# Kernel tuning notes

Hardware: AMD Instinct MI355X
Metric: run time of the kernel (lower is better)

The kernel has to match this reference:

```python
import jax, jax.numpy as jnp
import numpy as np

B, N, D, H = 4, 2048, 768, 12
HD = D // H
SCALE = HD ** -0.5


def setup_inputs() -> dict:
    key = jax.random.key(0)
    k1, k2, k3 = jax.random.split(key, 3)
    x = jax.random.normal(k1, (B, N, D), dtype=jnp.float32)
    w_qkv = jax.random.normal(k2, (D, 3 * D), dtype=jnp.float32) * (D ** -0.5)
    w_proj = jax.random.normal(k3, (D, D), dtype=jnp.float32) * (D ** -0.5)
    b_proj = jnp.zeros((D,), dtype=jnp.float32)
    return {"x": x, "w_qkv": w_qkv, "w_proj": w_proj, "b_proj": b_proj}


def reference(x, w_qkv, w_proj, b_proj):
    b, n, d = x.shape
    qkv = x @ w_qkv                      # [b, n, 3d]
    q, k, v = jnp.split(qkv, 3, axis=-1)
    # [b, n, d] -> [b, h, n, hd]
    split_heads = lambda t: t.reshape(b, n, H, HD).transpose(0, 2, 1, 3)
    q, k, v = split_heads(q), split_heads(k), split_heads(v)
    dots = jnp.einsum('bhqd,bhkd->bhqk', q, k) * SCALE   # [b, h, n, n]
    attn = jax.nn.softmax(dots, axis=-1)
    q_attn = attn[:, :, 0, :]            # attention row of query token 0: [b, h, n]
    # dropout p=0 (eval) -> identity
    out = jnp.einsum('bhqk,bhkd->bhqd', attn, v)          # [b, h, n, hd]
    out = out.transpose(0, 2, 1, 3).reshape(b, n, d)      # [b, n, d]
    return out @ w_proj + b_proj, q_attn
```

## Files before the change

kernel.cpp:

```cpp
#include <hip/hip_runtime.h>


typedef unsigned short u16;
typedef __attribute__((ext_vector_type(8))) short bf8;
typedef __attribute__((ext_vector_type(4))) short bf4;
typedef __attribute__((ext_vector_type(4))) int i4;
typedef __attribute__((ext_vector_type(4))) float f4;

#define MFMA16(a, b, c) __builtin_amdgcn_mfma_f32_16x16x32_bf16((a), (b), (c), 0, 0, 0)

#if __has_builtin(__builtin_amdgcn_exp2f)
#define EXP2(x) __builtin_amdgcn_exp2f(x)
#else
#define EXP2(x) __expf((x) * 0.6931471805599453f)
#endif

__device__ __forceinline__ float b2f(u16 h) {
  union { unsigned u; float f; } v; v.u = ((unsigned)h) << 16; return v.f;
}
__device__ __forceinline__ u16 f2b(float f) {
  union { float f; unsigned u; } v; v.f = f;
  unsigned r = v.u + 0x7fffu + ((v.u >> 16) & 1u);
  return (u16)(r >> 16);
}
__device__ __forceinline__ unsigned pack2(float a, float b) {
#if __has_builtin(__builtin_amdgcn_perm)
  return __builtin_amdgcn_perm(__builtin_bit_cast(unsigned, b),
                               __builtin_bit_cast(unsigned, a), 0x07060302u);
#else
  return (__builtin_bit_cast(unsigned, b) & 0xFFFF0000u) |
         (__builtin_bit_cast(unsigned, a) >> 16);
#endif
}
__device__ __forceinline__ void gload16(const u16* g, u16* l) {
  __builtin_amdgcn_global_load_lds(
      (const __attribute__((address_space(1))) void*)g,
      (__attribute__((address_space(3))) void*)l, 16, 0, 0);
}
__device__ __forceinline__ int detect_f32(const u16* x) {
  unsigned v = x[2 * (threadIdx.x & 63)];
  unsigned e = (v >> 7) & 0xFF;
  return __ballot(e >= 0x8E) != 0ull;
}

__global__ __launch_bounds__(256) void prep(
    const void* __restrict__ x, u16* __restrict__ xbf,
    const void* __restrict__ wqkv, u16* __restrict__ wqkvT,
    const void* __restrict__ wproj, u16* __restrict__ wprojT) {
  const int z = blockIdx.z;
  if (z == 2) {
    const int f32 = detect_f32((const u16*)x);
    const int lin = blockIdx.y * 72 + blockIdx.x;
    if (f32) {
      const float2* in = (const float2*)x;
      unsigned* out = (unsigned*)xbf;
      for (int i = lin * 256 + threadIdx.x; i < 3145728; i += 442368) {
        float2 v = in[i];
        out[i] = (unsigned)f2b(v.x) | ((unsigned)f2b(v.y) << 16);
      }
    } else {
      const unsigned* in = (const unsigned*)x;
      unsigned* out = (unsigned*)xbf;
      for (int i = lin * 256 + threadIdx.x; i < 3145728; i += 442368)
        out[i] = in[i];
    }
    return;
  }
  if (z == 1 && blockIdx.x >= 24) return;
  const void* in = z ? wproj : wqkv;
  u16* out = z ? wprojT : wqkvT;
  const int R = 768, C = z ? 768 : 2304;
  __shared__ u16 tile[32][33];
  const int f32 = detect_f32((const u16*)x);
  const int bx = blockIdx.x * 32, by = blockIdx.y * 32;
  const int tx = threadIdx.x & 31, ty = threadIdx.x >> 5;
#pragma unroll
  for (int i = 0; i < 4; i++) {
    size_t idx = (size_t)(by + ty + i * 8) * C + bx + tx;
    tile[ty + i * 8][tx] = f32 ? f2b(((const float*)in)[idx]) : ((const u16*)in)[idx];
  }
  __syncthreads();
#pragma unroll
  for (int i = 0; i < 4; i++)
    out[(size_t)(bx + ty + i * 8) * R + by + tx] = tile[tx][ty + i * 8];
}

template <int BIAS, int QATTN>
__global__ __launch_bounds__(256, 4) void gemm_bt(
    const u16* __restrict__ A, const u16* __restrict__ Bt,
    const void* __restrict__ bias, void* __restrict__ C,
    int M, int Ncols, int K, const u16* __restrict__ xdet,
    u16* __restrict__ Vt, const float* __restrict__ qe,
    const float* __restrict__ lout) {
  if (QATTN && blockIdx.x == 6) {
    const int f32o = detect_f32(xdet);
    const int base = blockIdx.y * 1536;
    for (int j = threadIdx.x; j < 1536; j += 256) {
      int idx = base + j;
      float v = qe[idx] * (1.f / lout[idx >> 11]);
      size_t oidx = (size_t)6291456 + idx;
      if (f32o) ((float*)C)[oidx] = v; else ((u16*)C)[oidx] = f2b(v);
    }
    return;
  }
  __shared__ alignas(16) u16 Al[2][128 * 32];
  __shared__ alignas(16) u16 Bl[2][128 * 32];
  const int t = threadIdx.x;
  const int lane = t & 63, wave = t >> 6;
  const int wr = wave >> 1, wc = wave & 1;
  const int quad = lane >> 4, l16 = lane & 15;
  const int bm = blockIdx.y * 128, bn = blockIdx.x * 128;
  const int f32o = BIAS ? detect_f32(xdet) : 0;
  const int grow = lane >> 2, gcol = (lane & 3) * 8;
  const int chunk0 = wave * 2, chunk1 = wave * 2 + 1;
  const int arow0 = chunk0 * 16 + grow, arow1 = chunk1 * 16 + grow;
  f4 acc[4][4] = {};
  gload16(A + (size_t)(bm + arow0) * K + gcol, &Al[0][chunk0 * 512]);
  gload16(Bt + (size_t)(bn + arow0) * K + gcol, &Bl[0][chunk0 * 512]);
  gload16(A + (size_t)(bm + arow1) * K + gcol, &Al[0][chunk1 * 512]);
  gload16(Bt + (size_t)(bn + arow1) * K + gcol, &Bl[0][chunk1 * 512]);
  const int NIT = K >> 5;
  for (int i = 0; i < NIT; i++) {
    const int cur = i & 1, nxt = cur ^ 1;
    __syncthreads();
    if (i + 1 < NIT) {
      int k0 = (i + 1) << 5;
      gload16(A + (size_t)(bm + arow0) * K + k0 + gcol, &Al[nxt][chunk0 * 512]);
      gload16(Bt + (size_t)(bn + arow0) * K + k0 + gcol, &Bl[nxt][chunk0 * 512]);
      gload16(A + (size_t)(bm + arow1) * K + k0 + gcol, &Al[nxt][chunk1 * 512]);
      gload16(Bt + (size_t)(bn + arow1) * K + k0 + gcol, &Bl[nxt][chunk1 * 512]);
    }
    bf8 af[4], bfr[4];
#pragma unroll
    for (int mt = 0; mt < 4; mt++)
      af[mt] = *(const bf8*)&Al[cur][(wr * 64 + mt * 16 + l16) * 32 + quad * 8];
#pragma unroll
    for (int nt = 0; nt < 4; nt++)
      bfr[nt] = *(const bf8*)&Bl[cur][(wc * 64 + nt * 16 + l16) * 32 + quad * 8];
#pragma unroll
    for (int mt = 0; mt < 4; mt++)
#pragma unroll
      for (int nt = 0; nt < 4; nt++)
        acc[mt][nt] = MFMA16(af[mt], bfr[nt], acc[mt][nt]);
  }
  if (Vt != nullptr && bn >= 1536) {
    const int b = bm >> 11;
#pragma unroll
    for (int mt = 0; mt < 4; mt++) {
      int n0 = (bm & 2047) + wr * 64 + mt * 16 + quad * 4;
      int n2 = (n0 & ~31) | (((n0 >> 2) & 3) << 3) | (((n0 >> 4) & 1) << 2);
#pragma unroll
      for (int nt = 0; nt < 4; nt++) {
        int colv = bn - 1536 + wc * 64 + nt * 16 + l16;
        int h = colv >> 6, d = colv & 63;
        bf4 pk = {(short)f2b(acc[mt][nt][0]), (short)f2b(acc[mt][nt][1]),
                  (short)f2b(acc[mt][nt][2]), (short)f2b(acc[mt][nt][3])};
        *(bf4*)&Vt[(size_t)((b * 12 + h) * 64 + d) * 2048 + n2] = pk;
      }
    }
    return;
  }
#pragma unroll
  for (int mt = 0; mt < 4; mt++) {
    int row = bm + wr * 64 + mt * 16 + quad * 4;
#pragma unroll
    for (int nt = 0; nt < 4; nt++) {
      int col = bn + wc * 64 + nt * 16 + l16;
      float bv = 0.f;
      if (BIAS)
        bv = f32o ? ((const float*)bias)[col] : b2f(((const u16*)bias)[col]);
#pragma unroll
      for (int r = 0; r < 4; r++) {
        size_t idx = (size_t)(row + r) * Ncols + col;
        float v = acc[mt][nt][r] + bv;
        if (f32o) ((float*)C)[idx] = v; else ((u16*)C)[idx] = f2b(v);
      }
    }
  }
}

__global__ __launch_bounds__(256, 3) void flash_attn(
    const u16* __restrict__ qkv, const u16* __restrict__ Vt,
    u16* __restrict__ O, float* __restrict__ qe, float* __restrict__ lout) {
  __shared__ alignas(16) u16 lds[3][8192];
  const int t = threadIdx.x, lane = t & 63, wave = t >> 6;
  const int quad = lane >> 4, l16 = lane & 15;
  const int id = blockIdx.x;
  const int bh = (id & 7) + 8 * (id >> 7);
  const int qtile = (id >> 3) & 15;
  const int b = bh / 12, h = bh - b * 12;
  const int q0 = qtile * 128 + wave * 32;
  const bool dumpP = (qe != nullptr) && (qtile == 0) && (wave == 0);
  const float SCALE2 = 0.125f * 1.44269504089f;
  const float mM0 = -16.f;
  bf8 qf[2][2];
#pragma unroll
  for (int qt = 0; qt < 2; qt++) {
    const u16* Qr = qkv + (size_t)(b * 2048 + q0 + qt * 16 + l16) * 2304 + h * 64;
    bf8 r0 = *(const bf8*)(Qr + quad * 8);
    bf8 r1 = *(const bf8*)(Qr + 32 + quad * 8);
#pragma unroll
    for (int j = 0; j < 8; j++) {
      qf[qt][0][j] = (short)f2b(b2f((u16)r0[j]) * SCALE2);
      qf[qt][1][j] = (short)f2b(b2f((u16)r1[j]) * SCALE2);
    }
  }
  bf8 ones;
#pragma unroll
  for (int j = 0; j < 8; j++) ones[j] = (short)0x3F80;
  const u16* Kb = qkv + (size_t)(b * 2048) * 2304 + 768 + h * 64;
  const u16* Vb = Vt + (size_t)((b * 12 + h) * 64) * 2048;
  const int drow = wave * 16 + (lane >> 2);
  const int dcol = ((lane & 3) ^ ((lane >> 3) & 3)) * 8;
  const int swz = (quad ^ ((l16 >> 1) & 3)) * 8;
  f4 o[2][4] = {};
  f4 lacc[2] = {};

#define STAGE(tile, buf)                                            \
  {                                                                 \
    int n1_ = (tile) * 64;                                          \
    const u16* Kt_ = Kb + (size_t)(n1_ + drow) * 2304 + dcol;       \
    const u16* Vr_ = Vb + (size_t)drow * 2048 + n1_ + dcol;         \
    u16* base_ = &lds[buf][wave * 512];                             \
    gload16(Kt_, base_);                                            \
    gload16(Kt_ + 32, base_ + 2048);                                \
    gload16(Vr_, base_ + 4096);                                     \
    gload16(Vr_ + 32, base_ + 6144);                                \
  }

  STAGE(0, 0);
  STAGE(1, 1);

  int cur = 0;
  for (int i = 0; i < 32; i++) {
    if (i < 31) {
      asm volatile("s_waitcnt vmcnt(4)" ::: "memory");
    } else {
      asm volatile("s_waitcnt vmcnt(0)" ::: "memory");
    }
    __builtin_amdgcn_s_barrier();
    if (i + 2 < 32) {
      int pre = cur + 2; if (pre >= 3) pre -= 3;
      STAGE(i + 2, pre);
    }
    const u16* K0 = &lds[cur][0];
    const u16* K1 = &lds[cur][2048];
    union { i4 i; bf8 b; } pf[2][2];
#pragma unroll
    for (int kt = 0; kt < 4; kt++) {
      bf8 kf0 = *(const bf8*)&K0[(kt * 16 + l16) * 32 + swz];
      bf8 kf1 = *(const bf8*)&K1[(kt * 16 + l16) * 32 + swz];
#pragma unroll
      for (int qt = 0; qt < 2; qt++) {
        f4 z = {mM0, mM0, mM0, mM0};
        z = MFMA16(kf0, qf[qt][0], z);
        z = MFMA16(kf1, qf[qt][1], z);
        float e0 = EXP2(z[0]);
        float e1 = EXP2(z[1]);
        float e2 = EXP2(z[2]);
        float e3 = EXP2(z[3]);
        if (qt == 0 && dumpP && l16 == 0) {
          f4 ev = {e0, e1, e2, e3};
          *(f4*)&qe[bh * 2048 + i * 64 + kt * 16 + quad * 4] = ev;
        }
        pf[qt][kt >> 1].i[(kt & 1) * 2 + 0] = (int)pack2(e0, e1);
        pf[qt][kt >> 1].i[(kt & 1) * 2 + 1] = (int)pack2(e2, e3);
      }
    }
#pragma unroll
    for (int pair = 0; pair < 2; pair++) {
      const u16* Vp = &lds[cur][4096 + pair * 2048];
      lacc[0] = MFMA16(ones, pf[0][pair].b, lacc[0]);
      lacc[1] = MFMA16(ones, pf[1][pair].b, lacc[1]);
#pragma unroll
      for (int nt = 0; nt < 4; nt++) {
        bf8 vf = *(const bf8*)&Vp[(nt * 16 + l16) * 32 + swz];
        o[0][nt] = MFMA16(vf, pf[0][pair].b, o[0][nt]);
        o[1][nt] = MFMA16(vf, pf[1][pair].b, o[1][nt]);
      }
    }
    cur = (cur == 2) ? 0 : cur + 1;
  }
#undef STAGE
#pragma unroll
  for (int qt = 0; qt < 2; qt++) {
    float l = lacc[qt][0];
    if (qt == 0 && dumpP && lane == 0) lout[bh] = l;
    float inv = 1.f / l;
    size_t row = (size_t)(b * 2048 + q0 + qt * 16 + l16) * 768 + h * 64;
#pragma unroll
    for (int nt = 0; nt < 4; nt++) {
      bf4 pk = {(short)f2b(o[qt][nt][0] * inv), (short)f2b(o[qt][nt][1] * inv),
                (short)f2b(o[qt][nt][2] * inv), (short)f2b(o[qt][nt][3] * inv)};
      *(bf4*)&O[row + nt * 16 + quad * 4] = pk;
    }
  }
}

__global__ __launch_bounds__(256) void qattn_row0(
    const u16* __restrict__ qkv, void* __restrict__ out,
    const u16* __restrict__ xdet) {
  const int bh = blockIdx.x, b = bh / 12, h = bh % 12;
  __shared__ float qs[64];
  __shared__ float sv[2048];
  __shared__ float red[8];
  const int t = threadIdx.x;
  const int f32o = detect_f32(xdet);
  if (t < 64) qs[t] = b2f(qkv[(size_t)(b * 2048) * 2304 + h * 64 + t]);
  __syncthreads();
  float lmax = -1e30f;
  for (int k = t; k < 2048; k += 256) {
    const u16* Kr = qkv + (size_t)(b * 2048 + k) * 2304 + 768 + h * 64;
    float acc = 0.f;
#pragma unroll
    for (int j = 0; j < 8; j++) {
      bf8 kv = *(const bf8*)(Kr + j * 8);
#pragma unroll
      for (int d = 0; d < 8; d++) acc += qs[j * 8 + d] * b2f((u16)kv[d]);
    }
    acc *= 0.125f;
    sv[k] = acc;
    lmax = fmaxf(lmax, acc);
  }
#pragma unroll
  for (int off = 32; off >= 1; off >>= 1) lmax = fmaxf(lmax, __shfl_xor(lmax, off, 64));
  if ((t & 63) == 0) red[t >> 6] = lmax;
  __syncthreads();
  const float bmax = fmaxf(fmaxf(red[0], red[1]), fmaxf(red[2], red[3]));
  float lsum = 0.f;
  for (int k = t; k < 2048; k += 256) {
    float e = __expf(sv[k] - bmax);
    sv[k] = e;
    lsum += e;
  }
#pragma unroll
  for (int off = 32; off >= 1; off >>= 1) lsum += __shfl_xor(lsum, off, 64);
  if ((t & 63) == 0) red[4 + (t >> 6)] = lsum;
  __syncthreads();
  const float inv = 1.f / (red[4] + red[5] + red[6] + red[7]);
  for (int k = t; k < 2048; k += 256) {
    size_t idx = (size_t)6291456 + (size_t)bh * 2048 + k;
    float v = sv[k] * inv;
    if (f32o) ((float*)out)[idx] = v; else ((u16*)out)[idx] = f2b(v);
  }
}

extern "C" void kernel_launch(void* const* d_in, const int* in_sizes, int n_in,
                              void* d_out, int out_size, void* d_ws, size_t ws_size,
                              hipStream_t stream) {
  const void* x_raw      = d_in[0];
  const void* w_qkv_raw  = d_in[1];
  const void* w_proj_raw = d_in[2];
  const void* b_proj_raw = d_in[3];
  const u16* xdet = (const u16*)x_raw;
  char* ws = (char*)d_ws;
  u16* xbf    = (u16*)(ws + 256);
  u16* wqkvT  = (u16*)(ws + 12583168);
  u16* wprojT = (u16*)(ws + 16122112);
  u16* qkv    = (u16*)(ws + 17301760);
  u16* Vt     = (u16*)(ws + 55050496);
  float* qe   = (float*)(ws + 67633408);
  float* lout = (float*)(ws + 68026624);
  u16* attn   = xbf;
  const bool fused = ws_size >= 68026816ull;

  prep<<<dim3(72, 24, 3), 256, 0, stream>>>(
      x_raw, xbf, w_qkv_raw, wqkvT, w_proj_raw, wprojT);
  gemm_bt<0, 0><<<dim3(18, 64), 256, 0, stream>>>(
      xbf, wqkvT, nullptr, qkv, 8192, 2304, 768, xdet, Vt, nullptr, nullptr);
  flash_attn<<<dim3(768), 256, 0, stream>>>(qkv, Vt, attn,
                                            fused ? qe : nullptr,
                                            fused ? lout : nullptr);
  if (fused) {
    gemm_bt<1, 1><<<dim3(7, 64), 256, 0, stream>>>(
        attn, wprojT, b_proj_raw, d_out, 8192, 768, 768, xdet, nullptr, qe, lout);
  } else {
    gemm_bt<1, 0><<<dim3(6, 64), 256, 0, stream>>>(
        attn, wprojT, b_proj_raw, d_out, 8192, 768, 768, xdet, nullptr, nullptr, nullptr);
    qattn_row0<<<dim3(48), 256, 0, stream>>>(qkv, d_out, xdet);
  }
}
```

Baseline: 213.4 us.

## Load V fragments directly to registers, keep only K staged in LDS

The attention kernel stops staging V tiles through shared memory. Each wave now loads its V MFMA fragments from global memory straight into registers, double-buffered across iterations, while K keeps the triple-buffered LDS pipeline. This halves LDS usage and removes the V LDS writes and reads, with vmcnt waits retuned to match. In exchange it adds register pressure from 16 bf8 fragments per thread, and every wave redundantly fetches the same V data from global memory or cache.

```diff
diff --git a/kernel.cpp b/kernel.cpp
--- a/kernel.cpp
+++ b/kernel.cpp
@@ -182,7 +182,7 @@
 __global__ __launch_bounds__(256, 3) void flash_attn(
     const u16* __restrict__ qkv, const u16* __restrict__ Vt,
     u16* __restrict__ O, float* __restrict__ qe, float* __restrict__ lout) {
-  __shared__ alignas(16) u16 lds[3][8192];
+  __shared__ alignas(16) u16 lds[3][4096];
   const int t = threadIdx.x, lane = t & 63, wave = t >> 6;
   const int quad = lane >> 4, l16 = lane & 15;
   const int id = blockIdx.x;
@@ -213,75 +213,85 @@
   const int drow = wave * 16 + (lane >> 2);
   const int dcol = ((lane & 3) ^ ((lane >> 3) & 3)) * 8;
   const int swz = (quad ^ ((l16 >> 1) & 3)) * 8;
+  const u16* Vl = Vb + (size_t)l16 * 2048 + quad * 8;
   f4 o[2][4] = {};
   f4 lacc[2] = {};
-
-#define STAGE(tile, buf)                                            \
+  bf8 va[8], vb_[8];
+
+#define STAGEK(tile, buf)                                           \
   {                                                                 \
-    int n1_ = (tile) * 64;                                          \
-    const u16* Kt_ = Kb + (size_t)(n1_ + drow) * 2304 + dcol;       \
-    const u16* Vr_ = Vb + (size_t)drow * 2048 + n1_ + dcol;         \
+    const u16* Kt_ = Kb + (size_t)((tile) * 64 + drow) * 2304 + dcol; \
     u16* base_ = &lds[buf][wave * 512];                             \
     gload16(Kt_, base_);                                            \
     gload16(Kt_ + 32, base_ + 2048);                                \
-    gload16(Vr_, base_ + 4096);                                     \
-    gload16(Vr_ + 32, base_ + 6144);                                \
-  }
-
-  STAGE(0, 0);
-  STAGE(1, 1);
-
-  int cur = 0;
-  for (int i = 0; i < 32; i++) {
-    if (i < 31) {
-      asm volatile("s_waitcnt vmcnt(4)" ::: "memory");
-    } else {
-      asm volatile("s_waitcnt vmcnt(0)" ::: "memory");
-    }
-    __builtin_amdgcn_s_barrier();
-    if (i + 2 < 32) {
-      int pre = cur + 2; if (pre >= 3) pre -= 3;
-      STAGE(i + 2, pre);
-    }
-    const u16* K0 = &lds[cur][0];
-    const u16* K1 = &lds[cur][2048];
-    union { i4 i; bf8 b; } pf[2][2];
-#pragma unroll
-    for (int kt = 0; kt < 4; kt++) {
-      bf8 kf0 = *(const bf8*)&K0[(kt * 16 + l16) * 32 + swz];
-      bf8 kf1 = *(const bf8*)&K1[(kt * 16 + l16) * 32 + swz];
-#pragma unroll
-      for (int qt = 0; qt < 2; qt++) {
-        f4 z = {mM0, mM0, mM0, mM0};
-        z = MFMA16(kf0, qf[qt][0], z);
-        z = MFMA16(kf1, qf[qt][1], z);
-        float e0 = EXP2(z[0]);
-        float e1 = EXP2(z[1]);
-        float e2 = EXP2(z[2]);
-        float e3 = EXP2(z[3]);
-        if (qt == 0 && dumpP && l16 == 0) {
-          f4 ev = {e0, e1, e2, e3};
-          *(f4*)&qe[bh * 2048 + i * 64 + kt * 16 + quad * 4] = ev;
-        }
-        pf[qt][kt >> 1].i[(kt & 1) * 2 + 0] = (int)pack2(e0, e1);
-        pf[qt][kt >> 1].i[(kt & 1) * 2 + 1] = (int)pack2(e2, e3);
-      }
-    }
-#pragma unroll
-    for (int pair = 0; pair < 2; pair++) {
-      const u16* Vp = &lds[cur][4096 + pair * 2048];
-      lacc[0] = MFMA16(ones, pf[0][pair].b, lacc[0]);
-      lacc[1] = MFMA16(ones, pf[1][pair].b, lacc[1]);
-#pragma unroll
-      for (int nt = 0; nt < 4; nt++) {
-        bf8 vf = *(const bf8*)&Vp[(nt * 16 + l16) * 32 + swz];
-        o[0][nt] = MFMA16(vf, pf[0][pair].b, o[0][nt]);
-        o[1][nt] = MFMA16(vf, pf[1][pair].b, o[1][nt]);
-      }
-    }
-    cur = (cur == 2) ? 0 : cur + 1;
-  }
-#undef STAGE
+  }
+#define LOADV(dst, tile)                                            \
+  {                                                                 \
+    int n1_ = (tile) * 64;                                          \
+    _Pragma("unroll")                                               \
+    for (int pn = 0; pn < 8; pn++)                                  \
+      dst[pn] = *(const bf8*)&Vl[(size_t)((pn >> 1) * 16) * 2048 +  \
+                                 n1_ + (pn & 1) * 32];              \
+  }
+#define ITER(i, VC, VN)                                                      \
+  {                                                                          \
+    asm volatile("s_waitcnt vmcnt(10)" ::: "memory");       \
+    __builtin_amdgcn_s_barrier();                                            \
+    __builtin_amdgcn_sched_barrier(0);                                       \
+    const int cb_ = (i) % 3;                                                 \
+    if ((i) + 2 < 32) STAGEK((i) + 2, ((i) + 2) % 3);                        \
+    const u16* K0_ = &lds[cb_][0];                                           \
+    const u16* K1_ = &lds[cb_][2048];                                        \
+    union { i4 iv; bf8 bv; } pf[2][2];                                       \
+    _Pragma("unroll")                                                        \
+    for (int kt = 0; kt < 4; kt++) {                                         \
+      bf8 kf0 = *(const bf8*)&K0_[(kt * 16 + l16) * 32 + swz];               \
+      bf8 kf1 = *(const bf8*)&K1_[(kt * 16 + l16) * 32 + swz];               \
+      _Pragma("unroll")                                                      \
+      for (int qt = 0; qt < 2; qt++) {                                       \
+        f4 z = {mM0, mM0, mM0, mM0};                                         \
+        z = MFMA16(kf0, qf[qt][0], z);                                       \
+        z = MFMA16(kf1, qf[qt][1], z);                                       \
+        float e0 = EXP2(z[0]);                                               \
+        float e1 = EXP2(z[1]);                                               \
+        float e2 = EXP2(z[2]);                                               \
+        float e3 = EXP2(z[3]);                                               \
+        if (qt == 0 && dumpP && l16 == 0) {                                  \
+          f4 ev = {e0, e1, e2, e3};                                          \
+          *(f4*)&qe[bh * 2048 + (i) * 64 + kt * 16 + quad * 4] = ev;         \
+        }                                                                    \
+        pf[qt][kt >> 1].iv[(kt & 1) * 2 + 0] = (int)pack2(e0, e1);           \
+        pf[qt][kt >> 1].iv[(kt & 1) * 2 + 1] = (int)pack2(e2, e3);           \
+      }                                                                      \
+    }                                                                        \
+        \
+    if ((i) < 30) { asm volatile("s_waitcnt vmcnt(2)" ::: "memory"); }       \
+    else { asm volatile("s_waitcnt vmcnt(0)" ::: "memory"); }                \
+    __builtin_amdgcn_sched_barrier(0);                                       \
+    if ((i) + 1 < 32) LOADV(VN, (i) + 1);                                    \
+    _Pragma("unroll")                                                        \
+    for (int pair = 0; pair < 2; pair++) {                                   \
+      lacc[0] = MFMA16(ones, pf[0][pair].bv, lacc[0]);                       \
+      lacc[1] = MFMA16(ones, pf[1][pair].bv, lacc[1]);                       \
+      _Pragma("unroll")                                                      \
+      for (int nt = 0; nt < 4; nt++) {                                       \
+        bf8 vf = VC[nt * 2 + pair];                                          \
+        o[0][nt] = MFMA16(vf, pf[0][pair].bv, o[0][nt]);                     \
+        o[1][nt] = MFMA16(vf, pf[1][pair].bv, o[1][nt]);                     \
+      }                                                                      \
+    }                                                                        \
+  }
+
+  STAGEK(0, 0);
+  STAGEK(1, 1);
+  LOADV(va, 0);
+  for (int it2 = 0; it2 < 16; it2++) {
+    ITER(it2 * 2, va, vb_);
+    ITER(it2 * 2 + 1, vb_, va);
+  }
+#undef ITER
+#undef LOADV
+#undef STAGEK
 #pragma unroll
   for (int qt = 0; qt < 2; qt++) {
     float l = lacc[qt][0];
```

Measured after the change: 258.4 us. 1.21x slower.

## Replace QKV GEMM with 256x288 tiled 8-wave kernel using double-buffered LDS

Applied to the files above, without the earlier changes.

Adds a dedicated QKV projection kernel with 512 threads and 256x288 output tiles. It double-buffers K=64 slabs in LDS with direct global-to-LDS loads and swizzled reads, and raises MFMA priority during the compute phase. The larger tile increases operand reuse per block and cuts the grid from 1152 to 256 blocks. It writes Q/K row-major and V transposed with a permuted column order in the epilogue. In exchange it uses about 136KB of LDS per block and many accumulator registers, which limits occupancy, and 256 blocks may leave the GPU's compute units poorly balanced.

```diff
diff --git a/kernel.cpp b/kernel.cpp
--- a/kernel.cpp
+++ b/kernel.cpp
@@ -83,6 +83,101 @@
 #pragma unroll
   for (int i = 0; i < 4; i++)
     out[(size_t)(bx + ty + i * 8) * R + by + tx] = tile[tx][ty + i * 8];
+}
+
+__global__ __launch_bounds__(512, 2) void gemm_qkv8(
+    const u16* __restrict__ A, const u16* __restrict__ Bt,
+    u16* __restrict__ Cq, u16* __restrict__ Vt) {
+  __shared__ alignas(16) u16 L[2][34816];
+  const int t = threadIdx.x;
+  const int lane = t & 63, wave = t >> 6;
+  const int wr = wave >> 1, wc = wave & 1;
+  const int quad = lane >> 4, l16 = lane & 15;
+  const int bm = blockIdx.y * 256, bn = blockIdx.x * 288;
+  const int dcol = ((lane & 3) ^ ((lane >> 3) & 3)) * 8;
+  const int swzU = (quad ^ ((l16 >> 1) & 3)) * 8;
+  const int drow = lane >> 2;
+  f4 acc[4][9] = {};
+
+#define STAGE_ALL(kt, buf)                                                   \
+  for (int c = wave; c < 68; c += 8) {                                       \
+    const int isB = c >= 32;                                                 \
+    const int cb = isB ? c - 32 : c;                                         \
+    const int kq_ = isB ? (cb >= 18 ? 1 : 0) : (cb >> 4);                    \
+    const int r16 = isB ? (cb - kq_ * 18) : (cb & 15);                       \
+    const u16* src = (isB ? Bt : A) +                                        \
+        (size_t)((isB ? bn : bm) + r16 * 16 + drow) * 768 +                  \
+        (kt) * 64 + kq_ * 32 + dcol;                                         \
+    u16* dst = &L[buf][(isB ? 16384 + kq_ * 9216 : kq_ * 8192) + r16 * 512]; \
+    gload16(src, dst);                                                       \
+  }
+
+  STAGE_ALL(0, 0);
+  asm volatile("s_waitcnt vmcnt(0)" ::: "memory");
+  __builtin_amdgcn_sched_barrier(0);
+  __builtin_amdgcn_s_barrier();
+  __builtin_amdgcn_sched_barrier(0);
+
+  for (int j = 0; j < 12; j++) {
+    const int buf = j & 1;
+    if (j + 1 < 12) STAGE_ALL(j + 1, buf ^ 1);
+    const u16* Lb = &L[buf][0];
+    bf8 af[4][2];
+#pragma unroll
+    for (int m = 0; m < 4; m++)
+#pragma unroll
+      for (int kq = 0; kq < 2; kq++)
+        af[m][kq] = *(const bf8*)&Lb[kq * 8192 +
+                                     (wr * 64 + m * 16 + l16) * 32 + swzU];
+#pragma unroll
+    for (int p = 0; p < 3; p++) {
+      bf8 bfr[3][2];
+#pragma unroll
+      for (int nn = 0; nn < 3; nn++)
+#pragma unroll
+        for (int kq = 0; kq < 2; kq++)
+          bfr[nn][kq] = *(const bf8*)&Lb[16384 + kq * 9216 +
+              (wc * 144 + (p * 3 + nn) * 16 + l16) * 32 + swzU];
+      __builtin_amdgcn_s_setprio(1);
+#pragma unroll
+      for (int nn = 0; nn < 3; nn++)
+#pragma unroll
+        for (int m = 0; m < 4; m++) {
+          acc[m][p * 3 + nn] = MFMA16(af[m][0], bfr[nn][0], acc[m][p * 3 + nn]);
+          acc[m][p * 3 + nn] = MFMA16(af[m][1], bfr[nn][1], acc[m][p * 3 + nn]);
+        }
+      __builtin_amdgcn_s_setprio(0);
+    }
+    if (j + 1 < 12) {
+      asm volatile("s_waitcnt vmcnt(0)" ::: "memory");
+      __builtin_amdgcn_sched_barrier(0);
+      __builtin_amdgcn_s_barrier();
+      __builtin_amdgcn_sched_barrier(0);
+    }
+  }
+#undef STAGE_ALL
+
+  const int b_ = bm >> 11;
+#pragma unroll
+  for (int m = 0; m < 4; m++) {
+    const int row0 = bm + wr * 64 + m * 16 + quad * 4;
+    const int n0 = row0 & 2047;
+    const int n2 = (n0 & ~31) | (((n0 >> 2) & 3) << 3) | (((n0 >> 4) & 1) << 2);
+#pragma unroll
+    for (int ni = 0; ni < 9; ni++) {
+      const int col = bn + wc * 144 + ni * 16 + l16;
+      if (col >= 1536) {
+        const int colv = col - 1536, h = colv >> 6, d = colv & 63;
+        bf4 pk = {(short)f2b(acc[m][ni][0]), (short)f2b(acc[m][ni][1]),
+                  (short)f2b(acc[m][ni][2]), (short)f2b(acc[m][ni][3])};
+        *(bf4*)&Vt[(size_t)((b_ * 12 + h) * 64 + d) * 2048 + n2] = pk;
+      } else {
+#pragma unroll
+        for (int r = 0; r < 4; r++)
+          Cq[(size_t)(row0 + r) * 2304 + col] = f2b(acc[m][ni][r]);
+      }
+    }
+  }
 }
 
 template <int BIAS, int QATTN>
@@ -366,8 +461,7 @@
 
   prep<<<dim3(72, 24, 3), 256, 0, stream>>>(
       x_raw, xbf, w_qkv_raw, wqkvT, w_proj_raw, wprojT);
-  gemm_bt<0, 0><<<dim3(18, 64), 256, 0, stream>>>(
-      xbf, wqkvT, nullptr, qkv, 8192, 2304, 768, xdet, Vt, nullptr, nullptr);
+  gemm_qkv8<<<dim3(8, 32), 512, 0, stream>>>(xbf, wqkvT, qkv, Vt);
   flash_attn<<<dim3(768), 256, 0, stream>>>(qkv, Vt, attn,
                                             fused ? qe : nullptr,
                                             fused ? lout : nullptr);
```

New measurement: 209.4 us. About the same (-1.9%).
